# Kernel tuning notes

Hardware: AMD Instinct MI355X
Metric: run time of the kernel (lower is better)

## Reference

```python
import jax, jax.numpy as jnp
import numpy as np

TOKENS, DIM, DIM_OUT, R, ALPHA = 8192, 4096, 4096, 16, 32
SCALE = ALPHA / R  # 2.0


def setup_inputs() -> dict:
    key = jax.random.key(0)
    k1, k2, k3, k4, k5 = jax.random.split(key, 5)
    x = jax.random.normal(k1, (TOKENS, DIM), dtype=jnp.float32)
    A = jax.random.normal(k2, (DIM, R), dtype=jnp.float32)
    B = jax.random.normal(k3, (R, DIM_OUT), dtype=jnp.float32) * 0.02
    W = jax.random.normal(k4, (DIM_OUT, DIM), dtype=jnp.float32) * 0.02  # base Linear weight
    b = jax.random.normal(k5, (DIM_OUT,), dtype=jnp.float32)
    return {"x": x, "A": A, "B": B, "W": W, "b": b}


def reference(x, A, B, W, b):
    # LoRA path: x @ (A @ B) * scale, computed in the efficient low-rank order
    # (mathematically identical to materializing the full-rank weight).
    lora = ((x @ A) @ B) * SCALE              # [tokens, dim_out]
    base = x @ W.T + b                         # wrapped base Linear forward
    return lora + base
```

## Files before the change

### kernel.cpp

```cpp
#include <hip/hip_runtime.h>
#include <hip/hip_bf16.h>
#include <stdint.h>

#define TOKENS   8192
#define DIM      4096
#define DIM_OUT  4096
#define LORA_R   16
#define LORA_SCALE 2.0f

typedef __bf16 bf16_t;
typedef __attribute__((ext_vector_type(8))) __bf16 bfrag;
typedef __attribute__((ext_vector_type(4))) float f32x4;

__device__ __forceinline__ void gload_lds16(const bf16_t* gsrc, bf16_t* ldst) {
    __builtin_amdgcn_global_load_lds(
        (const __attribute__((address_space(1))) uint32_t*)(const void*)gsrc,
        (__attribute__((address_space(3))) uint32_t*)(void*)ldst,
        16, 0, 0);
}

#define CAST_BLOCKS 2048
__global__ void prep_kernel(const float* __restrict__ x, bf16_t* __restrict__ xb,
                            const float* __restrict__ W, const float* __restrict__ A,
                            const float* __restrict__ B, bf16_t* __restrict__ Wt) {
    if (blockIdx.x < CAST_BLOCKS) {
        const int total = TOKENS * DIM / 8;
        for (int i = blockIdx.x * blockDim.x + threadIdx.x; i < total;
             i += CAST_BLOCKS * 256) {
            const float4* p = reinterpret_cast<const float4*>(x + (size_t)i * 8);
            float4 v0 = p[0], v1 = p[1];
            union { bf16_t o[8]; uint4 u; } pk;
            pk.o[0] = (bf16_t)v0.x; pk.o[1] = (bf16_t)v0.y;
            pk.o[2] = (bf16_t)v0.z; pk.o[3] = (bf16_t)v0.w;
            pk.o[4] = (bf16_t)v1.x; pk.o[5] = (bf16_t)v1.y;
            pk.o[6] = (bf16_t)v1.z; pk.o[7] = (bf16_t)v1.w;
            *reinterpret_cast<uint4*>(xb + (size_t)i * 8) = pk.u;
        }
    } else {
        int idx = (blockIdx.x - CAST_BLOCKS) * blockDim.x + threadIdx.x;
        int k0 = (idx & 511) << 3;
        int n0 = (idx >> 9) << 2;

        float bn[4][16];
#pragma unroll
        for (int r = 0; r < 16; ++r) {
            float4 bv = *reinterpret_cast<const float4*>(B + (size_t)r * DIM_OUT + n0);
            bn[0][r] = bv.x; bn[1][r] = bv.y; bn[2][r] = bv.z; bn[3][r] = bv.w;
        }
        float ab[4][8];
#pragma unroll
        for (int j = 0; j < 8; ++j) {
            const float4* ap = reinterpret_cast<const float4*>(A + (size_t)(k0 + j) * LORA_R);
            float4 a0 = ap[0], a1 = ap[1], a2 = ap[2], a3 = ap[3];
            float av[16] = {a0.x,a0.y,a0.z,a0.w,a1.x,a1.y,a1.z,a1.w,
                            a2.x,a2.y,a2.z,a2.w,a3.x,a3.y,a3.z,a3.w};
#pragma unroll
            for (int n = 0; n < 4; ++n) {
                float s = 0.f;
#pragma unroll
                for (int r = 0; r < 16; ++r) s += av[r] * bn[n][r];
                ab[n][j] = s;
            }
        }
#pragma unroll
        for (int n = 0; n < 4; ++n) {
            const float4* wp = reinterpret_cast<const float4*>(W + (size_t)(n0 + n) * DIM + k0);
            float4 w0 = wp[0], w1 = wp[1];
            float wv[8] = {w0.x,w0.y,w0.z,w0.w,w1.x,w1.y,w1.z,w1.w};
            union { bf16_t o[8]; uint4 u; } pk;
#pragma unroll
            for (int j = 0; j < 8; ++j) pk.o[j] = (bf16_t)(wv[j] + LORA_SCALE * ab[n][j]);
            *reinterpret_cast<uint4*>(Wt + (size_t)(n0 + n) * DIM + k0) = pk.u;
        }
    }
}

#define BM 256
#define BN 256
#define BK 64
#define MB_BLKS (TOKENS / BM)
#define NB_BLKS (DIM_OUT / BN)
#define NT      (DIM / BK)

#define SB0() __builtin_amdgcn_sched_barrier(0)
#define BAR() do { __builtin_amdgcn_s_barrier(); SB0(); } while (0)
#define VMWAIT_(n) asm volatile("s_waitcnt vmcnt(" #n ")" ::: "memory")
#define VMWAIT(n) VMWAIT_(n)

__global__ __launch_bounds__(512, 2) void gemm_kernel(
    const bf16_t* __restrict__ Xb, const bf16_t* __restrict__ Wt,
    const float* __restrict__ bias, float* __restrict__ C)
{
    __shared__ __align__(16) bf16_t sA[2][BM][BK];
    __shared__ __align__(16) bf16_t sB[2][BN][BK];

    const int nwg = MB_BLKS * NB_BLKS;
    int bid = blockIdx.x;
    int swz = (bid & 7) * (nwg >> 3) + (bid >> 3);
    int bm = swz / NB_BLKS;
    int bn = swz % NB_BLKS;

    const int tid  = threadIdx.x;
    const int lane = tid & 63;
    const int wid  = tid >> 6;
    const int wr   = wid >> 2;
    const int wc   = wid & 3;

    const int srow = tid >> 3;
    const int scol = (tid & 7) * 8;
    const int koff = (((tid & 7) ^ ((tid >> 3) & 7)) * 8);
    const bf16_t* Ag = Xb + (size_t)(bm * BM + srow) * DIM + koff;
    const bf16_t* Bg = Wt + (size_t)(bn * BN + srow) * DIM + koff;

#define STAGE_A(dd, kt) do { \
    const bf16_t* s_ = Ag + (size_t)(kt) * BK; \
    bf16_t* d_ = &sA[dd][srow][scol]; \
    gload_lds16(s_,                     d_); \
    gload_lds16(s_ + (size_t)64  * DIM, d_ + 64  * BK); \
    gload_lds16(s_ + (size_t)128 * DIM, d_ + 128 * BK); \
    gload_lds16(s_ + (size_t)192 * DIM, d_ + 192 * BK); \
} while (0)

#define STAGE_B(dd, kt) do { \
    const bf16_t* s_ = Bg + (size_t)(kt) * BK; \
    bf16_t* d_ = &sB[dd][srow][scol]; \
    gload_lds16(s_,                     d_); \
    gload_lds16(s_ + (size_t)64  * DIM, d_ + 64  * BK); \
    gload_lds16(s_ + (size_t)128 * DIM, d_ + 128 * BK); \
    gload_lds16(s_ + (size_t)192 * DIM, d_ + 192 * BK); \
} while (0)

    const int q     = lane & 7;
    const int kslot = lane >> 4;
    const int r15   = lane & 15;
    const int cK0   = ((kslot    ) ^ q) * 8;
    const int cK1   = ((kslot + 4) ^ q) * 8;
    const int arow0 = wr * 128 + r15;
    const int brow0 = wc * 64  + r15;

    f32x4 acc[8][4] = {};
    bfrag aLo[4][2], aHi[4][2], bLo[2][2], bHi[2][2];

#define READ_A4(dst, dd, mb) do { \
    _Pragma("unroll") \
    for (int m_ = 0; m_ < 4; ++m_) { \
        dst[m_][0] = *reinterpret_cast<const bfrag*>(&sA[dd][arow0 + (mb + m_) * 16][cK0]); \
        dst[m_][1] = *reinterpret_cast<const bfrag*>(&sA[dd][arow0 + (mb + m_) * 16][cK1]); \
    } \
} while (0)

#define READ_B2(dst, dd, nb) do { \
    _Pragma("unroll") \
    for (int n_ = 0; n_ < 2; ++n_) { \
        dst[n_][0] = *reinterpret_cast<const bfrag*>(&sB[dd][brow0 + (nb + n_) * 16][cK0]); \
        dst[n_][1] = *reinterpret_cast<const bfrag*>(&sB[dd][brow0 + (nb + n_) * 16][cK1]); \
    } \
} while (0)

#define MFMA_Q(Af, Bf, mb, nb) do { \
    __builtin_amdgcn_s_setprio(1); \
    _Pragma("unroll") \
    for (int m_ = 0; m_ < 4; ++m_) \
    _Pragma("unroll") \
    for (int n_ = 0; n_ < 2; ++n_) \
    _Pragma("unroll") \
    for (int ks_ = 0; ks_ < 2; ++ks_) \
        acc[mb + m_][nb + n_] = __builtin_amdgcn_mfma_f32_16x16x32_bf16( \
            Af[m_][ks_], Bf[n_][ks_], acc[mb + m_][nb + n_], 0, 0, 0); \
    __builtin_amdgcn_s_setprio(0); \
} while (0)

#define TILE3(d, ktn, S, NEXTQ, VM) do { \
     READ_A4(aHi, d, 4); if (S) STAGE_B(d, ktn); \
             SB0(); MFMA_Q(aLo, bHi, 0, 2); VMWAIT(VM); BAR(); \
     if (NEXTQ) READ_A4(aLo, (d) ^ 1, 0); if (S) STAGE_A(d, ktn); \
             SB0(); MFMA_Q(aHi, bHi, 4, 2); BAR(); \
     MFMA_Q(aHi, bLo, 4, 0); \
             if (NEXTQ) { \
                 READ_B2(bLo, (d) ^ 1, 0); READ_B2(bHi, (d) ^ 1, 2); \
                 MFMA_Q(aLo, bLo, 0, 0); \
             } \
             BAR(); \
} while (0)

    STAGE_A(0, 0); STAGE_B(0, 0);
    STAGE_B(1, 1); STAGE_A(1, 1);
    VMWAIT(8);
    BAR();
    READ_A4(aLo, 0, 0); READ_B2(bLo, 0, 0); READ_B2(bHi, 0, 2);
    SB0();
    MFMA_Q(aLo, bLo, 0, 0);
    BAR();

    for (int it = 0; it < NT / 2 - 1; ++it) {
        int kt0 = 2 * it;
        TILE3(0, kt0 + 2, true, true, 4);
        TILE3(1, kt0 + 3, true, true, 4);
    }
    TILE3(0, 0, false, true, 0);
    TILE3(1, 0, false, false, 0);

    int row0 = bm * BM + wr * 128 + (lane >> 4) * 4;
    int col0 = bn * BN + wc * 64 + r15;
#pragma unroll
    for (int n = 0; n < 4; ++n) {
        int c = col0 + n * 16;
        float bv = bias[c];
#pragma unroll
        for (int m = 0; m < 8; ++m) {
            int r = row0 + m * 16;
#pragma unroll
            for (int j = 0; j < 4; ++j)
                C[(size_t)(r + j) * DIM_OUT + c] = acc[m][n][j] + bv;
        }
    }
}

extern "C" void kernel_launch(void* const* d_in, const int* in_sizes, int n_in,
                              void* d_out, int out_size, void* d_ws, size_t ws_size,
                              hipStream_t stream) {
    const float* x = (const float*)d_in[0];
    const float* A = (const float*)d_in[1];
    const float* B = (const float*)d_in[2];
    const float* W = (const float*)d_in[3];
    const float* b = (const float*)d_in[4];
    float* out = (float*)d_out;

    bf16_t* xb = (bf16_t*)d_ws;
    bf16_t* Wt = (bf16_t*)((char*)d_ws + (size_t)TOKENS * DIM * 2);

    prep_kernel<<<CAST_BLOCKS + 2048, 256, 0, stream>>>(x, xb, W, A, B, Wt);
    gemm_kernel<<<MB_BLKS * NB_BLKS, 512, 0, stream>>>(xb, Wt, b, out);
}
```

Baseline: 325.4 us.

## Load B fragments directly from global into registers, bypassing LDS

Removes the shared-memory staging buffer for the weight operand. Each wave now loads its B MFMA fragments straight from global memory into registers at the end of each tile. The A operand still goes through LDS double buffering. This cuts LDS traffic and LDS footprint, but waves that share the same columns now load the same B data twice. It also exposes global-load latency right before the next tile's MFMAs, and the compiler's vmcnt waits may also drain the A prefetch.

```diff
diff --git a/kernel.cpp b/kernel.cpp
--- a/kernel.cpp
+++ b/kernel.cpp
@@ -92,7 +92,6 @@
     const float* __restrict__ bias, float* __restrict__ C)
 {
     __shared__ __align__(16) bf16_t sA[2][BM][BK];
-    __shared__ __align__(16) bf16_t sB[2][BN][BK];
 
     const int nwg = MB_BLKS * NB_BLKS;
     int bid = blockIdx.x;
@@ -110,7 +109,6 @@
     const int scol = (tid & 7) * 8;
     const int koff = (((tid & 7) ^ ((tid >> 3) & 7)) * 8);
     const bf16_t* Ag = Xb + (size_t)(bm * BM + srow) * DIM + koff;
-    const bf16_t* Bg = Wt + (size_t)(bn * BN + srow) * DIM + koff;
 
 #define STAGE_A(dd, kt) do { \
     const bf16_t* s_ = Ag + (size_t)(kt) * BK; \
@@ -121,22 +119,14 @@
     gload_lds16(s_ + (size_t)192 * DIM, d_ + 192 * BK); \
 } while (0)
 
-#define STAGE_B(dd, kt) do { \
-    const bf16_t* s_ = Bg + (size_t)(kt) * BK; \
-    bf16_t* d_ = &sB[dd][srow][scol]; \
-    gload_lds16(s_,                     d_); \
-    gload_lds16(s_ + (size_t)64  * DIM, d_ + 64  * BK); \
-    gload_lds16(s_ + (size_t)128 * DIM, d_ + 128 * BK); \
-    gload_lds16(s_ + (size_t)192 * DIM, d_ + 192 * BK); \
-} while (0)
-
     const int q     = lane & 7;
     const int kslot = lane >> 4;
     const int r15   = lane & 15;
     const int cK0   = ((kslot    ) ^ q) * 8;
     const int cK1   = ((kslot + 4) ^ q) * 8;
     const int arow0 = wr * 128 + r15;
-    const int brow0 = wc * 64  + r15;
+
+    const bf16_t* Bgl = Wt + (size_t)(bn * BN + wc * 64 + r15) * DIM + kslot * 8;
 
     f32x4 acc[8][4] = {};
     bfrag aLo[4][2], aHi[4][2], bLo[2][2], bHi[2][2];
@@ -149,11 +139,12 @@
     } \
 } while (0)
 
-#define READ_B2(dst, dd, nb) do { \
+#define GLOAD_B2(dst, nb, ktb) do { \
     _Pragma("unroll") \
     for (int n_ = 0; n_ < 2; ++n_) { \
-        dst[n_][0] = *reinterpret_cast<const bfrag*>(&sB[dd][brow0 + (nb + n_) * 16][cK0]); \
-        dst[n_][1] = *reinterpret_cast<const bfrag*>(&sB[dd][brow0 + (nb + n_) * 16][cK1]); \
+        const bf16_t* p_ = Bgl + (size_t)((nb) + n_) * 16 * DIM + (size_t)(ktb) * BK; \
+        dst[n_][0] = *reinterpret_cast<const bfrag*>(p_); \
+        dst[n_][1] = *reinterpret_cast<const bfrag*>(p_ + 32); \
     } \
 } while (0)
 
@@ -170,35 +161,31 @@
     __builtin_amdgcn_s_setprio(0); \
 } while (0)
 
-#define TILE3(d, ktn, S, NEXTQ, VM) do { \
-     READ_A4(aHi, d, 4); if (S) STAGE_B(d, ktn); \
-             SB0(); MFMA_Q(aLo, bHi, 0, 2); VMWAIT(VM); BAR(); \
-     if (NEXTQ) READ_A4(aLo, (d) ^ 1, 0); if (S) STAGE_A(d, ktn); \
+#define TILE(d, kta, ktb, S, NEXT) do { \
+     READ_A4(aHi, d, 4); \
+             SB0(); MFMA_Q(aLo, bLo, 0, 0); BAR(); \
+     if (S) STAGE_A(d, kta); \
+             SB0(); MFMA_Q(aLo, bHi, 0, 2); BAR(); \
+     if (NEXT) READ_A4(aLo, (d) ^ 1, 0); \
              SB0(); MFMA_Q(aHi, bHi, 4, 2); BAR(); \
      MFMA_Q(aHi, bLo, 4, 0); \
-             if (NEXTQ) { \
-                 READ_B2(bLo, (d) ^ 1, 0); READ_B2(bHi, (d) ^ 1, 2); \
-                 MFMA_Q(aLo, bLo, 0, 0); \
-             } \
+             if (NEXT) { GLOAD_B2(bLo, 0, ktb); GLOAD_B2(bHi, 2, ktb); } \
              BAR(); \
 } while (0)
 
-    STAGE_A(0, 0); STAGE_B(0, 0);
-    STAGE_B(1, 1); STAGE_A(1, 1);
-    VMWAIT(8);
+    STAGE_A(0, 0); STAGE_A(1, 1);
+    GLOAD_B2(bLo, 0, 0); GLOAD_B2(bHi, 2, 0);
+    VMWAIT(12);
     BAR();
-    READ_A4(aLo, 0, 0); READ_B2(bLo, 0, 0); READ_B2(bHi, 0, 2);
-    SB0();
-    MFMA_Q(aLo, bLo, 0, 0);
-    BAR();
+    READ_A4(aLo, 0, 0);
 
     for (int it = 0; it < NT / 2 - 1; ++it) {
         int kt0 = 2 * it;
-        TILE3(0, kt0 + 2, true, true, 4);
-        TILE3(1, kt0 + 3, true, true, 4);
+        TILE(0, kt0 + 2, kt0 + 1, true, true);
+        TILE(1, kt0 + 3, kt0 + 2, true, true);
     }
-    TILE3(0, 0, false, true, 0);
-    TILE3(1, 0, false, false, 0);
+    TILE(0, 0, 63, false, true);
+    TILE(1, 0, 0,  false, false);
 
     int row0 = bm * BM + wr * 128 + (lane >> 4) * 4;
     int col0 = bn * BN + wc * 64 + r15;
```

New measurement: 484.8 us. 49.0% more time.

## Replace interleaved three-barrier tile pipeline with simple one-barrier double-buffered loop

Applied to the files above, without the earlier changes.

Replaces the hand-scheduled pipeline, which interleaved LDS reads, MFMA quarters and prefetches across three barriers per K-tile, with a plain double-buffered loop. Each tile now issues the next tile's global-to-LDS loads, reads all fragments, runs all MFMAs, then waits for every outstanding load and takes one barrier. This cuts barriers per tile and simplifies the code, but the full vmcnt(0) wait at the end of each tile exposes global load latency that the old schedule hid, and MFMA no longer overlaps the LDS fragment reads.

```diff
diff --git a/kernel.cpp b/kernel.cpp
--- a/kernel.cpp
+++ b/kernel.cpp
@@ -83,9 +83,9 @@
 #define NT      (DIM / BK)
 
 #define SB0() __builtin_amdgcn_sched_barrier(0)
-#define BAR() do { __builtin_amdgcn_s_barrier(); SB0(); } while (0)
 #define VMWAIT_(n) asm volatile("s_waitcnt vmcnt(" #n ")" ::: "memory")
 #define VMWAIT(n) VMWAIT_(n)
+#define TILEBAR() do { SB0(); VMWAIT(0); __builtin_amdgcn_s_barrier(); SB0(); } while (0)
 
 __global__ __launch_bounds__(512, 2) void gemm_kernel(
     const bf16_t* __restrict__ Xb, const bf16_t* __restrict__ Wt,
@@ -170,35 +170,24 @@
     __builtin_amdgcn_s_setprio(0); \
 } while (0)
 
-#define TILE3(d, ktn, S, NEXTQ, VM) do { \
-     READ_A4(aHi, d, 4); if (S) STAGE_B(d, ktn); \
-             SB0(); MFMA_Q(aLo, bHi, 0, 2); VMWAIT(VM); BAR(); \
-     if (NEXTQ) READ_A4(aLo, (d) ^ 1, 0); if (S) STAGE_A(d, ktn); \
-             SB0(); MFMA_Q(aHi, bHi, 4, 2); BAR(); \
-     MFMA_Q(aHi, bLo, 4, 0); \
-             if (NEXTQ) { \
-                 READ_B2(bLo, (d) ^ 1, 0); READ_B2(bHi, (d) ^ 1, 2); \
-                 MFMA_Q(aLo, bLo, 0, 0); \
-             } \
-             BAR(); \
+#define TILE1(d, ktn, S) do { \
+    if (S) { STAGE_A((d) ^ 1, ktn); STAGE_B((d) ^ 1, ktn); } \
+    READ_A4(aLo, d, 0); READ_B2(bLo, d, 0); READ_B2(bHi, d, 2); READ_A4(aHi, d, 4); \
+    MFMA_Q(aLo, bLo, 0, 0); MFMA_Q(aLo, bHi, 0, 2); \
+    MFMA_Q(aHi, bHi, 4, 2); MFMA_Q(aHi, bLo, 4, 0); \
+    TILEBAR(); \
 } while (0)
 
     STAGE_A(0, 0); STAGE_B(0, 0);
-    STAGE_B(1, 1); STAGE_A(1, 1);
-    VMWAIT(8);
-    BAR();
-    READ_A4(aLo, 0, 0); READ_B2(bLo, 0, 0); READ_B2(bHi, 0, 2);
-    SB0();
-    MFMA_Q(aLo, bLo, 0, 0);
-    BAR();
+    TILEBAR();
 
     for (int it = 0; it < NT / 2 - 1; ++it) {
-        int kt0 = 2 * it;
-        TILE3(0, kt0 + 2, true, true, 4);
-        TILE3(1, kt0 + 3, true, true, 4);
+        int t = 2 * it;
+        TILE1(0, t + 1, true);
+        TILE1(1, t + 2, true);
     }
-    TILE3(0, 0, false, true, 0);
-    TILE3(1, 0, false, false, 0);
+    TILE1(0, 63, true);
+    TILE1(1, 0, false);
 
     int row0 = bm * BM + wr * 128 + (lane >> 4) * 4;
     int col0 = bn * BN + wc * 64 + r15;
```

Result: slower. 335.7 us (+3.2%).
